# Kernel optimization log

Measured on AMD Instinct MI355X. Metric: run time of the kernel, lower is better.

## Reference

```python
import jax, jax.numpy as jnp
import numpy as np

B, S, C, H = 64, 512, 256, 128
P = S  # predict_length defaults to seq_length


def _linear_init(k, fan_in, fan_out):
    bound = 1.0 / np.sqrt(fan_in)
    kw, kb = jax.random.split(k)
    w = jax.random.uniform(kw, (fan_in, fan_out), minval=-bound, maxval=bound, dtype=jnp.float32)
    b = jax.random.uniform(kb, (fan_out,), minval=-bound, maxval=bound, dtype=jnp.float32)
    return w, b


def setup_inputs() -> dict:
    key = jax.random.key(0)
    ks = jax.random.split(key, 10)
    x = jax.random.normal(ks[0], (B, S, C), dtype=jnp.float32)
    wq1, bq1 = _linear_init(ks[1], S, H)
    wk1, bk1 = _linear_init(ks[2], S, H)
    wq2, bq2 = _linear_init(ks[3], S // 2, H)
    wk2, bk2 = _linear_init(ks[4], S // 2, H)
    wq3, bq3 = _linear_init(ks[5], S // 4, H)
    wk3, bk3 = _linear_init(ks[6], S // 4, H)
    wv, bv = _linear_init(ks[7], S, S)
    wo, bo = _linear_init(ks[8], S, P)
    return dict(x=x, wq1=wq1, bq1=bq1, wk1=wk1, bk1=bk1,
                wq2=wq2, bq2=bq2, wk2=wk2, bk2=bk2,
                wq3=wq3, bq3=bq3, wk3=wk3, bk3=bk3,
                wv=wv, bv=bv, wo=wo, bo=bo)


def _channel_attn(xl, wq, bq, wk, bk):
    # xl: [b', C, L]; q,k: [b', C, H]; returns softmax channel-attention [b', C, C]
    q = xl @ wq + bq
    k = xl @ wk + bk
    scores = jnp.einsum('bch,bdh->bcd', q, k) / jnp.sqrt(jnp.asarray(H, q.dtype))
    return jax.nn.softmax(scores, axis=-1)


def reference(x, wq1, bq1, wk1, bk1, wq2, bq2, wk2, bk2, wq3, bq3, wk3, bk3, wv, bv, wo, bo):
    b, s, c = x.shape
    x1 = jnp.swapaxes(x, -2, -1)                                   # [B, C, S]
    x2 = jnp.swapaxes(x.reshape(b * 2, s // 2, c), -2, -1)          # [2B, C, S/2]
    x3 = jnp.swapaxes(x.reshape(b * 4, s // 4, c), -2, -1)          # [4B, C, S/4]
    a1 = _channel_attn(x1, wq1, bq1, wk1, bk1)                      # [B, C, C]
    a2 = _channel_attn(x2, wq2, bq2, wk2, bk2).reshape(b, 2, c, c).mean(axis=1)
    a3 = _channel_attn(x3, wq3, bq3, wk3, bk3).reshape(b, 4, c, c).mean(axis=1)
    stacked = jnp.stack([a1, a2, a3], axis=0)                       # [3, B, C, C]
    gate = jax.nn.softmax(stacked, axis=0)                          # softmax over scales
    attn = (stacked * gate).sum(axis=0)                             # gated multi-scale combine [B, C, C]
    v = x1 @ wv + bv                                                # [B, C, S]
    out = (attn @ v) @ wo + bo                                      # [B, C, P]
    return jnp.swapaxes(out, -2, -1)                                # [B, P, C]
```

## Files before the change

### kernel.cpp

```cpp
#include <hip/hip_runtime.h>
#include <hip/hip_bf16.h>


typedef __attribute__((ext_vector_type(8))) short bf16x8;
typedef __attribute__((ext_vector_type(4))) float f32x4;
typedef __attribute__((ext_vector_type(8))) unsigned short ushort8;

typedef __attribute__((address_space(1))) void* as1vp;
typedef __attribute__((address_space(3))) void* as3vp;

__device__ __forceinline__ void gl2lds16(const void* g, void* l) {
  __builtin_amdgcn_global_load_lds((as1vp)(void*)g, (as3vp)l, 16, 0, 0);
}

__device__ __forceinline__ float bf2f(unsigned short u) {
  union { unsigned int i; float f; } v; v.i = ((unsigned int)u) << 16; return v.f;
}
__device__ __forceinline__ unsigned short f2bf(float f) {
  union { float f; unsigned int i; } v; v.f = f;
  unsigned int r = v.i + 0x7FFFu + ((v.i >> 16) & 1u);
  return (unsigned short)(r >> 16);
}
__device__ __forceinline__ unsigned long long pack4bf(float a, float b, float c, float d) {
  return (unsigned long long)f2bf(a) | ((unsigned long long)f2bf(b) << 16) |
         ((unsigned long long)f2bf(c) << 32) | ((unsigned long long)f2bf(d) << 48);
}

__global__ void __launch_bounds__(256) tcast_all(
    const float* __restrict__ x,
    const float* __restrict__ wq1, const float* __restrict__ wk1,
    const float* __restrict__ wq2, const float* __restrict__ wk2,
    const float* __restrict__ wq3, const float* __restrict__ wk3,
    const float* __restrict__ wv, const float* __restrict__ wo,
    unsigned short* __restrict__ XT,
    unsigned short* __restrict__ W1, unsigned short* __restrict__ W2,
    unsigned short* __restrict__ W3, unsigned short* __restrict__ WVNT,
    unsigned short* __restrict__ WOT) {
  const int bid = blockIdx.x;
  const int t = threadIdx.x;
  if (bid >= 2168) {
    long i0 = (long)(bid - 2168) * 2048 + t * 8;
    f32x4 a = *(const f32x4*)(wv + i0);
    f32x4 b = *(const f32x4*)(wv + i0 + 4);
    ushort8 o;
#pragma unroll
    for (int j = 0; j < 4; ++j) { o[j] = f2bf(a[j]); o[4 + j] = f2bf(b[j]); }
    *(ushort8*)(WVNT + i0) = o;
    return;
  }
  __shared__ float lds[64][68];
  const float* S; unsigned short* D; int R, Cc, r0, c0, rowoff = 0;
  if (bid < 2048) {
    int bz = bid >> 5, i = bid & 31;
    S = x + (long)bz * 131072; D = XT + (long)bz * 131072;
    R = 512; Cc = 256; r0 = (i & 7) * 64; c0 = (i >> 3) * 64;
  } else {
    int wb = bid - 2048;
    if (wb < 32) {
      int m = wb >> 4, i = wb & 15;
      S = m ? wk1 : wq1; D = W1; R = 512; Cc = 128;
      r0 = (i & 7) * 64; c0 = (i >> 3) * 64; rowoff = m * 128;
    } else if (wb < 48) {
      int m = (wb - 32) >> 3, i = (wb - 32) & 7;
      S = m ? wk2 : wq2; D = W2; R = 256; Cc = 128;
      r0 = (i & 3) * 64; c0 = (i >> 2) * 64; rowoff = m * 128;
    } else if (wb < 56) {
      int m = (wb - 48) >> 2, i = (wb - 48) & 3;
      S = m ? wk3 : wq3; D = W3; R = 128; Cc = 128;
      r0 = (i & 1) * 64; c0 = (i >> 1) * 64; rowoff = m * 128;
    } else {
      int i = wb - 56; S = wo; D = WOT; R = 512; Cc = 512;
      r0 = (i & 7) * 64; c0 = (i >> 3) * 64;
    }
  }
  {
    const int row = t >> 2, cq = (t & 3) * 16;
    const float* Sp = S + (long)(r0 + row) * Cc + c0 + cq;
#pragma unroll
    for (int j = 0; j < 4; ++j)
      *(f32x4*)&lds[row][cq + j * 4] = *(const f32x4*)(Sp + j * 4);
  }
  __syncthreads();
  {
    const int rq = (t & 15) * 4, ccb = t >> 4;
#pragma unroll
    for (int j = 0; j < 4; ++j) {
      int cc = ccb + j * 16;
      *(unsigned long long*)(D + (long)(c0 + cc + rowoff) * R + r0 + rq) =
          pack4bf(lds[rq][cc], lds[rq + 1][cc], lds[rq + 2][cc], lds[rq + 3][cc]);
    }
  }
}

__global__ void __launch_bounds__(512) projscore(
    const unsigned short* __restrict__ XT,
    const unsigned short* __restrict__ W1, const unsigned short* __restrict__ W2,
    const unsigned short* __restrict__ W3,
    const unsigned short* __restrict__ WOT, const unsigned short* __restrict__ WVNT,
    unsigned short* __restrict__ WVOT, float* __restrict__ BVO,
    const float* __restrict__ bv,
    unsigned short* __restrict__ A1F, unsigned short* __restrict__ A2F,
    unsigned short* __restrict__ A3F,
    const float* __restrict__ bq1, const float* __restrict__ bk1,
    const float* __restrict__ bq2, const float* __restrict__ bk2,
    const float* __restrict__ bq3, const float* __restrict__ bk3) {
  extern __shared__ char smem[];
  const int z = blockIdx.z;
  const int t = threadIdx.x, lane = t & 63, wid = t >> 6;

  if (z >= 464) {
    int p0 = (z - 464) * 128 + wid * 16;
    f32x4 b0 = *(const f32x4*)(bv + lane * 8);
    f32x4 b1 = *(const f32x4*)(bv + lane * 8 + 4);
#pragma unroll
    for (int i = 0; i < 16; ++i) {
      int p = p0 + i;
      bf16x8 wrow = *(const bf16x8*)(WOT + (long)p * 512 + lane * 8);
      float s = 0.0f;
#pragma unroll
      for (int j = 0; j < 4; ++j) {
        s += b0[j] * bf2f((unsigned short)wrow[j]);
        s += b1[j] * bf2f((unsigned short)wrow[4 + j]);
      }
#pragma unroll
      for (int off = 1; off < 64; off <<= 1) s += __shfl_xor(s, off, 64);
      if (lane == 0) BVO[p] = s;
    }
    return;
  }

  const int srow = t >> 3, ssl = t & 7;

  if (z >= 448) {
    const int w = z - 448;
    const int m0 = (w >> 2) * 128, n0 = (w & 3) * 128;
    const unsigned short* Ab = WOT + (long)m0 * 512;
    const unsigned short* Bb = WVNT + (long)n0 * 512;
    const int wmb = (wid >> 2) * 64, wnb = (wid & 3) * 32;
    f32x4 acc[4][2] = {};
    auto stageS = [&](int buf, int k0) {
      char* s = smem + buf * 32768;
#pragma unroll
      for (int i = 0; i < 2; ++i) {
        int row = i * 64 + srow;
        gl2lds16(Ab + (long)row * 512 + k0 + (ssl ^ (row & 7)) * 8, s + i * 8192 + t * 16);
        gl2lds16(Bb + (long)row * 512 + k0 + (ssl ^ (row & 7)) * 8, s + 16384 + i * 8192 + t * 16);
      }
    };
    stageS(0, 0);
    stageS(1, 64);
    for (int j = 0; j < 8; ++j) {
      if (j < 7) asm volatile("s_waitcnt vmcnt(4)" ::: "memory");
      else       asm volatile("s_waitcnt vmcnt(0)" ::: "memory");
      __builtin_amdgcn_s_barrier();
      if (j + 2 < 8) stageS((j + 2) % 3, (j + 2) * 64);
      const char* s = smem + (j % 3) * 32768;
#pragma unroll
      for (int kk = 0; kk < 2; ++kk) {
        const int slot = kk * 4 + (lane >> 4);
        bf16x8 af[4], bfr[2];
#pragma unroll
        for (int mi = 0; mi < 4; ++mi) {
          int row = wmb + mi * 16 + (lane & 15);
          af[mi] = *(const bf16x8*)(s + row * 128 + 16 * (slot ^ (row & 7)));
        }
#pragma unroll
        for (int ni = 0; ni < 2; ++ni) {
          int row = wnb + ni * 16 + (lane & 15);
          bfr[ni] = *(const bf16x8*)(s + 16384 + row * 128 + 16 * (slot ^ (row & 7)));
        }
#pragma unroll
        for (int mi = 0; mi < 4; ++mi)
#pragma unroll
          for (int ni = 0; ni < 2; ++ni)
            acc[mi][ni] = __builtin_amdgcn_mfma_f32_16x16x32_bf16(af[mi], bfr[ni], acc[mi][ni], 0, 0, 0);
      }
    }
#pragma unroll
    for (int ni = 0; ni < 2; ++ni) {
      int col = n0 + wnb + ni * 16 + (lane & 15);
#pragma unroll
      for (int mi = 0; mi < 4; ++mi) {
        int rowb = m0 + wmb + mi * 16 + (lane >> 4) * 4;
#pragma unroll
        for (int r = 0; r < 4; ++r)
          WVOT[(long)(rowb + r) * 512 + col] = f2bf(acc[mi][ni][r]);
      }
    }
    return;
  }

  const unsigned short* Ab; const unsigned short* Bw; unsigned short* AF;
  const float *bq, *bk; int K; long sb;
  if (z < 64) {
    K = 512; Bw = W1; AF = A1F; sb = z; bq = bq1; bk = bk1;
    Ab = XT + (long)z * 131072;
  } else if (z < 192) {
    int u = z - 64; K = 256; Bw = W2; AF = A2F; sb = u; bq = bq2; bk = bk2;
    Ab = XT + (long)(u >> 1) * 131072 + (u & 1) * 256;
  } else {
    int u = z - 192; K = 128; Bw = W3; AF = A3F; sb = u; bq = bq3; bk = bk3;
    Ab = XT + (long)(u >> 2) * 131072 + (u & 3) * 128;
  }
  const int wmb = (wid >> 1) * 64, wnb = (wid & 1) * 128;

  auto stage = [&](int buf, int k0) {
    char* s = smem + buf * 65536;
#pragma unroll
    for (int i = 0; i < 4; ++i) {
      int row = i * 64 + srow;
      int sc = (ssl ^ (row & 7)) * 8;
      gl2lds16(Ab + (long)row * 512 + k0 + sc, s + i * 8192 + t * 16);
      gl2lds16(Bw + (long)row * K + k0 + sc, s + 32768 + i * 8192 + t * 16);
    }
  };

  f32x4 acc[4][8] = {};
  const int nst = K >> 6;
  stage(0, 0);
  __syncthreads();
  int cur = 0;
  for (int j = 0; j < nst; ++j) {
    if (j + 1 < nst) stage(cur ^ 1, (j + 1) * 64);
    const char* s = smem + cur * 65536;
#pragma unroll
    for (int kk = 0; kk < 2; ++kk) {
      const int slot = kk * 4 + (lane >> 4);
      bf16x8 af[4], bfr[8];
#pragma unroll
      for (int mi = 0; mi < 4; ++mi) {
        int row = wmb + mi * 16 + (lane & 15);
        af[mi] = *(const bf16x8*)(s + row * 128 + 16 * (slot ^ (row & 7)));
      }
#pragma unroll
      for (int ni = 0; ni < 8; ++ni) {
        int row = wnb + ni * 16 + (lane & 15);
        bfr[ni] = *(const bf16x8*)(s + 32768 + row * 128 + 16 * (slot ^ (row & 7)));
      }
#pragma unroll
      for (int mi = 0; mi < 4; ++mi)
#pragma unroll
        for (int ni = 0; ni < 8; ++ni)
          acc[mi][ni] = __builtin_amdgcn_mfma_f32_16x16x32_bf16(bfr[ni], af[mi], acc[mi][ni], 0, 0, 0);
    }
    __syncthreads();
    cur ^= 1;
  }

  {
    const int chB = (wid & 1) ? 65536 : 0;
    const float* bias = (wid & 1) ? bk : bq;
#pragma unroll
    for (int mi = 0; mi < 4; ++mi) {
      int rowm = wmb + mi * 16 + (lane & 15);
#pragma unroll
      for (int ni = 0; ni < 8; ++ni) {
        int h = ni * 16 + (lane >> 4) * 4;
        int addr = chB + (h >> 6) * 32768 + rowm * 128 +
                   16 * ((((h & 63) >> 3)) ^ (rowm & 7)) + (h & 7) * 2;
        *(unsigned long long*)(smem + addr) =
            pack4bf(acc[mi][ni][0] + bias[h], acc[mi][ni][1] + bias[h + 1],
                    acc[mi][ni][2] + bias[h + 2], acc[mi][ni][3] + bias[h + 3]);
      }
    }
  }
  __syncthreads();

  f32x4 acc2[2][16] = {};
#pragma unroll
  for (int kc = 0; kc < 2; ++kc)
#pragma unroll
    for (int kk = 0; kk < 2; ++kk) {
      const int slot = kk * 4 + (lane >> 4);
      bf16x8 qf[2];
#pragma unroll
      for (int m2 = 0; m2 < 2; ++m2) {
        int qrow = wid * 32 + m2 * 16 + (lane & 15);
        qf[m2] = *(const bf16x8*)(smem + kc * 32768 + qrow * 128 + 16 * (slot ^ (qrow & 7)));
      }
#pragma unroll
      for (int ni = 0; ni < 16; ++ni) {
        int krow = ni * 16 + (lane & 15);
        bf16x8 kf = *(const bf16x8*)(smem + 65536 + kc * 32768 + krow * 128 + 16 * (slot ^ (krow & 7)));
        acc2[0][ni] = __builtin_amdgcn_mfma_f32_16x16x32_bf16(qf[0], kf, acc2[0][ni], 0, 0, 0);
        acc2[1][ni] = __builtin_amdgcn_mfma_f32_16x16x32_bf16(qf[1], kf, acc2[1][ni], 0, 0, 0);
      }
    }

  const float sc = 0.088388347648318447f;
#pragma unroll
  for (int m2 = 0; m2 < 2; ++m2) {
    int quad = (2 * wid + m2) & 3;
    int m0idx = (2 * wid + m2) >> 2;
    unsigned short* Of = AF + ((sb * 4 + m0idx) * 256 + quad * 64 + lane) * 64;
#pragma unroll
    for (int r = 0; r < 4; ++r) {
      float mx = -1e30f;
#pragma unroll
      for (int ni = 0; ni < 16; ++ni) mx = fmaxf(mx, acc2[m2][ni][r]);
#pragma unroll
      for (int off = 1; off < 16; off <<= 1) mx = fmaxf(mx, __shfl_xor(mx, off, 64));
      float s = 0.0f;
#pragma unroll
      for (int ni = 0; ni < 16; ++ni) {
        float p = __expf((acc2[m2][ni][r] - mx) * sc);
        acc2[m2][ni][r] = p;
        s += p;
      }
#pragma unroll
      for (int off = 1; off < 16; off <<= 1) s += __shfl_xor(s, off, 64);
      float inv = 1.0f / s;
      ushort8 lo, hi;
#pragma unroll
      for (int j = 0; j < 8; ++j) {
        lo[j] = f2bf(acc2[m2][j][r] * inv);
        hi[j] = f2bf(acc2[m2][8 + j][r] * inv);
      }
      *(ushort8*)(Of + r * 16) = lo;
      *(ushort8*)(Of + r * 16 + 8) = hi;
    }
  }
}

__global__ void __launch_bounds__(256) gate_frag(
    const unsigned short* __restrict__ A1F, const unsigned short* __restrict__ A2F,
    const unsigned short* __restrict__ A3F, unsigned short* __restrict__ ATTN) {
  const long gid = (long)blockIdx.x * 256 + threadIdx.x;
  const long i = gid * 8;
  const int b = (int)(i >> 16);
  const int rest = (int)(i & 65535);
  ushort8 a1 = *(const ushort8*)(A1F + i);
  const long i2 = ((long)(2 * b) << 16) + rest;
  ushort8 a2a = *(const ushort8*)(A2F + i2);
  ushort8 a2b = *(const ushort8*)(A2F + i2 + 65536);
  const long i3 = ((long)(4 * b) << 16) + rest;
  ushort8 a3a = *(const ushort8*)(A3F + i3);
  ushort8 a3b = *(const ushort8*)(A3F + i3 + 65536);
  ushort8 a3c = *(const ushort8*)(A3F + i3 + 131072);
  ushort8 a3d = *(const ushort8*)(A3F + i3 + 196608);
  const int f = rest & 63;
  const int tl = (rest >> 6) & 255;
  const int m0idx = rest >> 14;
  const int quad = (tl >> 6) & 3;
  const int lane_s = tl & 63;
  const int r = f >> 4;
  const int u0 = f & 15;
  const int row = m0idx * 64 + quad * 16 + (lane_s >> 4) * 4 + r;
  unsigned short* Orow = ATTN + ((long)b << 16) + (long)row * 256 + (lane_s & 15);
#pragma unroll
  for (int j = 0; j < 8; ++j) {
    float A1 = bf2f(a1[j]);
    float A2 = 0.5f * (bf2f(a2a[j]) + bf2f(a2b[j]));
    float A3 = 0.25f * (bf2f(a3a[j]) + bf2f(a3b[j]) + bf2f(a3c[j]) + bf2f(a3d[j]));
    float m = fmaxf(A1, fmaxf(A2, A3));
    float e1 = __expf(A1 - m), e2 = __expf(A2 - m), e3 = __expf(A3 - m);
    Orow[(u0 + j) * 16] = f2bf((A1 * e1 + A2 * e2 + A3 * e3) / (e1 + e2 + e3));
  }
}

template <int F32OUT, int BIASMODE>
__global__ void __launch_bounds__(512) gemm8(
    const unsigned short* __restrict__ A, const unsigned short* __restrict__ B,
    void* __restrict__ OutV, const float* __restrict__ bias,
    int lda, int ldb, int K, long astr, long bstr, long ostr, int ldo) {
  extern __shared__ char smem[];
  const int t = threadIdx.x, lane = t & 63, wid = t >> 6;
  const int wmb = (wid >> 1) * 64, wnb = (wid & 1) * 64;
  const int m0 = blockIdx.y * 256, n0 = blockIdx.x * 128;
  const int bz = blockIdx.z;
  const unsigned short* Ab = A + (long)bz * astr + (long)m0 * lda;
  const unsigned short* Bb = B + (long)bz * bstr + (long)n0 * ldb;
  const int srow = t >> 3, ssl = t & 7;

  auto stage = [&](int buf, int k0) {
    char* s = smem + buf * 49152;
#pragma unroll
    for (int i = 0; i < 4; ++i) {
      int row = i * 64 + srow;
      gl2lds16(Ab + (long)row * lda + k0 + (ssl ^ (row & 7)) * 8, s + i * 8192 + t * 16);
    }
#pragma unroll
    for (int i = 0; i < 2; ++i) {
      int row = i * 64 + srow;
      gl2lds16(Bb + (long)row * ldb + k0 + (ssl ^ (row & 7)) * 8,
               s + 32768 + i * 8192 + t * 16);
    }
  };

  f32x4 acc[4][4] = {};
  const int nst = K >> 6;
  stage(0, 0);
  stage(1, 64);
  for (int j = 0; j < nst; ++j) {
    if (j + 1 < nst) asm volatile("s_waitcnt vmcnt(6)" ::: "memory");
    else             asm volatile("s_waitcnt vmcnt(0)" ::: "memory");
    __builtin_amdgcn_s_barrier();
    if (j + 2 < nst) stage((j + 2) % 3, (j + 2) * 64);
    const char* s = smem + (j % 3) * 49152;
#pragma unroll
    for (int kk = 0; kk < 2; ++kk) {
      const int slot = kk * 4 + (lane >> 4);
      bf16x8 af[4], bfr[4];
#pragma unroll
      for (int mi = 0; mi < 4; ++mi) {
        int row = wmb + mi * 16 + (lane & 15);
        af[mi] = *(const bf16x8*)(s + row * 128 + 16 * (slot ^ (row & 7)));
      }
#pragma unroll
      for (int ni = 0; ni < 4; ++ni) {
        int row = wnb + ni * 16 + (lane & 15);
        bfr[ni] = *(const bf16x8*)(s + 32768 + row * 128 + 16 * (slot ^ (row & 7)));
      }
#pragma unroll
      for (int mi = 0; mi < 4; ++mi)
#pragma unroll
        for (int ni = 0; ni < 4; ++ni)
          acc[mi][ni] = __builtin_amdgcn_mfma_f32_16x16x32_bf16(af[mi], bfr[ni], acc[mi][ni], 0, 0, 0);
    }
  }
#pragma unroll
  for (int mi = 0; mi < 4; ++mi) {
    int rowb = m0 + wmb + mi * 16 + (lane >> 4) * 4;
    float rb[4];
#pragma unroll
    for (int r = 0; r < 4; ++r) rb[r] = (BIASMODE == 2) ? bias[rowb + r] : 0.0f;
#pragma unroll
    for (int ni = 0; ni < 4; ++ni) {
      int col = n0 + wnb + ni * 16 + (lane & 15);
#pragma unroll
      for (int r = 0; r < 4; ++r) {
        float v = acc[mi][ni][r] + rb[r];
        if constexpr (F32OUT)
          ((float*)OutV)[(long)bz * ostr + (long)(rowb + r) * ldo + col] = v;
        else
          ((unsigned short*)OutV)[(long)bz * ostr + (long)(rowb + r) * ldo + col] = f2bf(v);
      }
    }
  }
}

extern "C" void kernel_launch(void* const* d_in, const int* in_sizes, int n_in,
                              void* d_out, int out_size, void* d_ws, size_t ws_size,
                              hipStream_t stream) {
  (void)in_sizes; (void)n_in; (void)out_size; (void)ws_size;
  const float* x   = (const float*)d_in[0];
  const float* wq1 = (const float*)d_in[1];
  const float* bq1 = (const float*)d_in[2];
  const float* wk1 = (const float*)d_in[3];
  const float* bk1 = (const float*)d_in[4];
  const float* wq2 = (const float*)d_in[5];
  const float* bq2 = (const float*)d_in[6];
  const float* wk2 = (const float*)d_in[7];
  const float* bk2 = (const float*)d_in[8];
  const float* wq3 = (const float*)d_in[9];
  const float* bq3 = (const float*)d_in[10];
  const float* wk3 = (const float*)d_in[11];
  const float* bk3 = (const float*)d_in[12];
  const float* wv  = (const float*)d_in[13];
  const float* bv  = (const float*)d_in[14];
  const float* wo  = (const float*)d_in[15];
  const float* bo  = (const float*)d_in[16];
  char* ws = (char*)d_ws;

  unsigned short* XT   = (unsigned short*)(ws + 0);
  unsigned short* WQK1 = (unsigned short*)(ws + 16777216);
  unsigned short* WQK2 = (unsigned short*)(ws + 17039360);
  unsigned short* WQK3 = (unsigned short*)(ws + 17170432);
  unsigned short* WOT  = (unsigned short*)(ws + 17235968);
  unsigned short* WVNT = (unsigned short*)(ws + 17760256);
  unsigned short* WVOT = (unsigned short*)(ws + 18284544);
  float*          BVO  = (float*)(ws + 18808832);
  unsigned short* A1F  = (unsigned short*)(ws + 18876416);
  unsigned short* A2F  = (unsigned short*)(ws + 27265024);
  unsigned short* A3F  = (unsigned short*)(ws + 44042240);
  unsigned short* ATTN = (unsigned short*)(ws + 77596672);
  unsigned short* XVT  = (unsigned short*)(ws + 18876416);

  tcast_all<<<dim3(2296), dim3(256), 0, stream>>>(
      x, wq1, wk1, wq2, wk2, wq3, wk3, wv, wo,
      XT, WQK1, WQK2, WQK3, WVNT, WOT);

  projscore<<<dim3(1, 1, 468), dim3(512), 131072, stream>>>(
      XT, WQK1, WQK2, WQK3, WOT, WVNT, WVOT, BVO, bv,
      A1F, A2F, A3F, bq1, bk1, bq2, bk2, bq3, bk3);

  gate_frag<<<dim3(2048), dim3(256), 0, stream>>>(A1F, A2F, A3F, ATTN);

  gemm8<0, 2><<<dim3(2, 2, 64), dim3(512), 147456, stream>>>(
      WVOT, XT, XVT, BVO, 512, 512, 512, 0, 131072, 131072, 256);
  gemm8<1, 2><<<dim3(2, 2, 64), dim3(512), 147456, stream>>>(
      XVT, ATTN, d_out, bo, 256, 256, 256, 131072, 65536, 131072, 256);
}
```

Before: 95.48 us.

## Load B-operand fragments directly from global memory instead of staging through LDS

In the projscore kernel paths and in gemm8, the B operand is no longer copied into shared memory. Each lane reads its bf16x8 MFMA fragment straight from global memory (served by L1/L2), and the LDS buffers and waitcnt counts shrink to match. The goal is to halve LDS traffic and footprint, which could allow more blocks per CU. The cost is direct global loads in the inner loop whose latency is not hidden by the async prefetch pipeline, and the access pattern is poorly coalesced.

```diff
diff --git a/kernel.cpp b/kernel.cpp
--- a/kernel.cpp
+++ b/kernel.cpp
@@ -139,22 +139,19 @@
     const int wmb = (wid >> 2) * 64, wnb = (wid & 3) * 32;
     f32x4 acc[4][2] = {};
     auto stageS = [&](int buf, int k0) {
-      char* s = smem + buf * 32768;
+      char* s = smem + buf * 16384;
 #pragma unroll
       for (int i = 0; i < 2; ++i) {
         int row = i * 64 + srow;
         gl2lds16(Ab + (long)row * 512 + k0 + (ssl ^ (row & 7)) * 8, s + i * 8192 + t * 16);
-        gl2lds16(Bb + (long)row * 512 + k0 + (ssl ^ (row & 7)) * 8, s + 16384 + i * 8192 + t * 16);
       }
     };
     stageS(0, 0);
-    stageS(1, 64);
-    for (int j = 0; j < 8; ++j) {
-      if (j < 7) asm volatile("s_waitcnt vmcnt(4)" ::: "memory");
-      else       asm volatile("s_waitcnt vmcnt(0)" ::: "memory");
-      __builtin_amdgcn_s_barrier();
-      if (j + 2 < 8) stageS((j + 2) % 3, (j + 2) * 64);
-      const char* s = smem + (j % 3) * 32768;
+    __syncthreads();
+    int cur = 0;
+    for (int k0 = 0; k0 < 512; k0 += 64) {
+      if (k0 + 64 < 512) stageS(cur ^ 1, k0 + 64);
+      const char* s = smem + cur * 16384;
 #pragma unroll
       for (int kk = 0; kk < 2; ++kk) {
         const int slot = kk * 4 + (lane >> 4);
@@ -167,7 +164,7 @@
 #pragma unroll
         for (int ni = 0; ni < 2; ++ni) {
           int row = wnb + ni * 16 + (lane & 15);
-          bfr[ni] = *(const bf16x8*)(s + 16384 + row * 128 + 16 * (slot ^ (row & 7)));
+          bfr[ni] = *(const bf16x8*)(Bb + (long)row * 512 + k0 + slot * 8);
         }
 #pragma unroll
         for (int mi = 0; mi < 4; ++mi)
@@ -175,6 +172,8 @@
           for (int ni = 0; ni < 2; ++ni)
             acc[mi][ni] = __builtin_amdgcn_mfma_f32_16x16x32_bf16(af[mi], bfr[ni], acc[mi][ni], 0, 0, 0);
       }
+      __syncthreads();
+      cur ^= 1;
     }
 #pragma unroll
     for (int ni = 0; ni < 2; ++ni) {
@@ -205,13 +204,11 @@
   const int wmb = (wid >> 1) * 64, wnb = (wid & 1) * 128;
 
   auto stage = [&](int buf, int k0) {
-    char* s = smem + buf * 65536;
+    char* s = smem + buf * 32768;
 #pragma unroll
     for (int i = 0; i < 4; ++i) {
       int row = i * 64 + srow;
-      int sc = (ssl ^ (row & 7)) * 8;
-      gl2lds16(Ab + (long)row * 512 + k0 + sc, s + i * 8192 + t * 16);
-      gl2lds16(Bw + (long)row * K + k0 + sc, s + 32768 + i * 8192 + t * 16);
+      gl2lds16(Ab + (long)row * 512 + k0 + (ssl ^ (row & 7)) * 8, s + i * 8192 + t * 16);
     }
   };
 
@@ -222,7 +219,8 @@
   int cur = 0;
   for (int j = 0; j < nst; ++j) {
     if (j + 1 < nst) stage(cur ^ 1, (j + 1) * 64);
-    const char* s = smem + cur * 65536;
+    const int k0 = j * 64;
+    const char* s = smem + cur * 32768;
 #pragma unroll
     for (int kk = 0; kk < 2; ++kk) {
       const int slot = kk * 4 + (lane >> 4);
@@ -235,7 +233,7 @@
 #pragma unroll
       for (int ni = 0; ni < 8; ++ni) {
         int row = wnb + ni * 16 + (lane & 15);
-        bfr[ni] = *(const bf16x8*)(s + 32768 + row * 128 + 16 * (slot ^ (row & 7)));
+        bfr[ni] = *(const bf16x8*)(Bw + (long)row * K + k0 + slot * 8);
       }
 #pragma unroll
       for (int mi = 0; mi < 4; ++mi)
@@ -373,17 +371,11 @@
   const int srow = t >> 3, ssl = t & 7;
 
   auto stage = [&](int buf, int k0) {
-    char* s = smem + buf * 49152;
+    char* s = smem + buf * 32768;
 #pragma unroll
     for (int i = 0; i < 4; ++i) {
       int row = i * 64 + srow;
       gl2lds16(Ab + (long)row * lda + k0 + (ssl ^ (row & 7)) * 8, s + i * 8192 + t * 16);
-    }
-#pragma unroll
-    for (int i = 0; i < 2; ++i) {
-      int row = i * 64 + srow;
-      gl2lds16(Bb + (long)row * ldb + k0 + (ssl ^ (row & 7)) * 8,
-               s + 32768 + i * 8192 + t * 16);
     }
   };
 
@@ -392,11 +384,12 @@
   stage(0, 0);
   stage(1, 64);
   for (int j = 0; j < nst; ++j) {
-    if (j + 1 < nst) asm volatile("s_waitcnt vmcnt(6)" ::: "memory");
+    if (j + 1 < nst) asm volatile("s_waitcnt vmcnt(4)" ::: "memory");
     else             asm volatile("s_waitcnt vmcnt(0)" ::: "memory");
     __builtin_amdgcn_s_barrier();
     if (j + 2 < nst) stage((j + 2) % 3, (j + 2) * 64);
-    const char* s = smem + (j % 3) * 49152;
+    const int k0 = j * 64;
+    const char* s = smem + (j % 3) * 32768;
 #pragma unroll
     for (int kk = 0; kk < 2; ++kk) {
       const int slot = kk * 4 + (lane >> 4);
@@ -409,7 +402,7 @@
 #pragma unroll
       for (int ni = 0; ni < 4; ++ni) {
         int row = wnb + ni * 16 + (lane & 15);
-        bfr[ni] = *(const bf16x8*)(s + 32768 + row * 128 + 16 * (slot ^ (row & 7)));
+        bfr[ni] = *(const bf16x8*)(Bb + (long)row * ldb + k0 + slot * 8);
       }
 #pragma unroll
       for (int mi = 0; mi < 4; ++mi)
@@ -486,8 +479,8 @@
 
   gate_frag<<<dim3(2048), dim3(256), 0, stream>>>(A1F, A2F, A3F, ATTN);
 
-  gemm8<0, 2><<<dim3(2, 2, 64), dim3(512), 147456, stream>>>(
+  gemm8<0, 2><<<dim3(2, 2, 64), dim3(512), 98304, stream>>>(
       WVOT, XT, XVT, BVO, 512, 512, 512, 0, 131072, 131072, 256);
-  gemm8<1, 2><<<dim3(2, 2, 64), dim3(512), 147456, stream>>>(
+  gemm8<1, 2><<<dim3(2, 2, 64), dim3(512), 98304, stream>>>(
       XVT, ATTN, d_out, bo, 256, 256, 256, 131072, 65536, 131072, 256);
 }
```

Result: slower. 130.2 us (+36.4%).

## Run projscore with 1024-thread blocks to halve per-wave tiles and registers

Applied to the files above, without the earlier changes.

Doubles the projscore block to 16 waves and shrinks each wave's accumulator tiles (projection 4x4, score one 16-row strip, WV·WO subblock 2x2). The aim is more waves in flight per CU to hide MFMA and LDS latency, and lower register pressure per wave. The WV·WO path also loses its triple-buffered pipelined staging in favour of a single buffer with a barrier each k-step, which may expose load latency. Larger blocks also mean more costly barriers.

```diff
diff --git a/kernel.cpp b/kernel.cpp
--- a/kernel.cpp
+++ b/kernel.cpp
@@ -92,7 +92,7 @@
   }
 }
 
-__global__ void __launch_bounds__(512) projscore(
+__global__ void __launch_bounds__(1024) projscore(
     const unsigned short* __restrict__ XT,
     const unsigned short* __restrict__ W1, const unsigned short* __restrict__ W2,
     const unsigned short* __restrict__ W3,
@@ -109,11 +109,11 @@
   const int t = threadIdx.x, lane = t & 63, wid = t >> 6;
 
   if (z >= 464) {
-    int p0 = (z - 464) * 128 + wid * 16;
+    int p0 = (z - 464) * 128 + wid * 8;
     f32x4 b0 = *(const f32x4*)(bv + lane * 8);
     f32x4 b1 = *(const f32x4*)(bv + lane * 8 + 4);
 #pragma unroll
-    for (int i = 0; i < 16; ++i) {
+    for (int i = 0; i < 8; ++i) {
       int p = p0 + i;
       bf16x8 wrow = *(const bf16x8*)(WOT + (long)p * 512 + lane * 8);
       float s = 0.0f;
@@ -129,58 +129,47 @@
     return;
   }
 
-  const int srow = t >> 3, ssl = t & 7;
+  const int rS = t >> 3, sS = t & 7;
 
   if (z >= 448) {
     const int w = z - 448;
     const int m0 = (w >> 2) * 128, n0 = (w & 3) * 128;
     const unsigned short* Ab = WOT + (long)m0 * 512;
     const unsigned short* Bb = WVNT + (long)n0 * 512;
-    const int wmb = (wid >> 2) * 64, wnb = (wid & 3) * 32;
-    f32x4 acc[4][2] = {};
-    auto stageS = [&](int buf, int k0) {
-      char* s = smem + buf * 32768;
-#pragma unroll
-      for (int i = 0; i < 2; ++i) {
-        int row = i * 64 + srow;
-        gl2lds16(Ab + (long)row * 512 + k0 + (ssl ^ (row & 7)) * 8, s + i * 8192 + t * 16);
-        gl2lds16(Bb + (long)row * 512 + k0 + (ssl ^ (row & 7)) * 8, s + 16384 + i * 8192 + t * 16);
-      }
-    };
-    stageS(0, 0);
-    stageS(1, 64);
-    for (int j = 0; j < 8; ++j) {
-      if (j < 7) asm volatile("s_waitcnt vmcnt(4)" ::: "memory");
-      else       asm volatile("s_waitcnt vmcnt(0)" ::: "memory");
-      __builtin_amdgcn_s_barrier();
-      if (j + 2 < 8) stageS((j + 2) % 3, (j + 2) * 64);
-      const char* s = smem + (j % 3) * 32768;
+    const int wmb = (wid >> 2) * 32, wnb = (wid & 3) * 32;
+    f32x4 acc[2][2] = {};
+    for (int k0 = 0; k0 < 512; k0 += 64) {
+      int sc = (sS ^ (rS & 7)) * 8;
+      gl2lds16(Ab + (long)rS * 512 + k0 + sc, smem + t * 16);
+      gl2lds16(Bb + (long)rS * 512 + k0 + sc, smem + 16384 + t * 16);
+      __syncthreads();
 #pragma unroll
       for (int kk = 0; kk < 2; ++kk) {
         const int slot = kk * 4 + (lane >> 4);
-        bf16x8 af[4], bfr[2];
-#pragma unroll
-        for (int mi = 0; mi < 4; ++mi) {
+        bf16x8 af[2], bfr[2];
+#pragma unroll
+        for (int mi = 0; mi < 2; ++mi) {
           int row = wmb + mi * 16 + (lane & 15);
-          af[mi] = *(const bf16x8*)(s + row * 128 + 16 * (slot ^ (row & 7)));
+          af[mi] = *(const bf16x8*)(smem + row * 128 + 16 * (slot ^ (row & 7)));
         }
 #pragma unroll
         for (int ni = 0; ni < 2; ++ni) {
           int row = wnb + ni * 16 + (lane & 15);
-          bfr[ni] = *(const bf16x8*)(s + 16384 + row * 128 + 16 * (slot ^ (row & 7)));
+          bfr[ni] = *(const bf16x8*)(smem + 16384 + row * 128 + 16 * (slot ^ (row & 7)));
         }
 #pragma unroll
-        for (int mi = 0; mi < 4; ++mi)
+        for (int mi = 0; mi < 2; ++mi)
 #pragma unroll
           for (int ni = 0; ni < 2; ++ni)
             acc[mi][ni] = __builtin_amdgcn_mfma_f32_16x16x32_bf16(af[mi], bfr[ni], acc[mi][ni], 0, 0, 0);
       }
+      __syncthreads();
     }
 #pragma unroll
     for (int ni = 0; ni < 2; ++ni) {
       int col = n0 + wnb + ni * 16 + (lane & 15);
 #pragma unroll
-      for (int mi = 0; mi < 4; ++mi) {
+      for (int mi = 0; mi < 2; ++mi) {
         int rowb = m0 + wmb + mi * 16 + (lane >> 4) * 4;
 #pragma unroll
         for (int r = 0; r < 4; ++r)
@@ -202,20 +191,20 @@
     int u = z - 192; K = 128; Bw = W3; AF = A3F; sb = u; bq = bq3; bk = bk3;
     Ab = XT + (long)(u >> 2) * 131072 + (u & 3) * 128;
   }
-  const int wmb = (wid >> 1) * 64, wnb = (wid & 1) * 128;
+  const int wmb = (wid >> 2) * 64, wnb = (wid & 3) * 64;
 
   auto stage = [&](int buf, int k0) {
     char* s = smem + buf * 65536;
 #pragma unroll
-    for (int i = 0; i < 4; ++i) {
-      int row = i * 64 + srow;
-      int sc = (ssl ^ (row & 7)) * 8;
-      gl2lds16(Ab + (long)row * 512 + k0 + sc, s + i * 8192 + t * 16);
-      gl2lds16(Bw + (long)row * K + k0 + sc, s + 32768 + i * 8192 + t * 16);
+    for (int i = 0; i < 2; ++i) {
+      int row = i * 128 + rS;
+      int sc = (sS ^ (row & 7)) * 8;
+      gl2lds16(Ab + (long)row * 512 + k0 + sc, s + i * 16384 + t * 16);
+      gl2lds16(Bw + (long)row * K + k0 + sc, s + 32768 + i * 16384 + t * 16);
     }
   };
 
-  f32x4 acc[4][8] = {};
+  f32x4 acc[4][4] = {};
   const int nst = K >> 6;
   stage(0, 0);
   __syncthreads();
@@ -226,21 +215,21 @@
 #pragma unroll
     for (int kk = 0; kk < 2; ++kk) {
       const int slot = kk * 4 + (lane >> 4);
-      bf16x8 af[4], bfr[8];
+      bf16x8 af[4], bfr[4];
 #pragma unroll
       for (int mi = 0; mi < 4; ++mi) {
         int row = wmb + mi * 16 + (lane & 15);
         af[mi] = *(const bf16x8*)(s + row * 128 + 16 * (slot ^ (row & 7)));
       }
 #pragma unroll
-      for (int ni = 0; ni < 8; ++ni) {
+      for (int ni = 0; ni < 4; ++ni) {
         int row = wnb + ni * 16 + (lane & 15);
         bfr[ni] = *(const bf16x8*)(s + 32768 + row * 128 + 16 * (slot ^ (row & 7)));
       }
 #pragma unroll
       for (int mi = 0; mi < 4; ++mi)
 #pragma unroll
-        for (int ni = 0; ni < 8; ++ni)
+        for (int ni = 0; ni < 4; ++ni)
           acc[mi][ni] = __builtin_amdgcn_mfma_f32_16x16x32_bf16(bfr[ni], af[mi], acc[mi][ni], 0, 0, 0);
     }
     __syncthreads();
@@ -248,16 +237,17 @@
   }
 
   {
-    const int chB = (wid & 1) ? 65536 : 0;
-    const float* bias = (wid & 1) ? bk : bq;
+    const int chB = (wnb < 128) ? 0 : 65536;
+    const float* bias = (wnb < 128) ? bq : bk;
+    const int hbase = wnb & 127;
 #pragma unroll
     for (int mi = 0; mi < 4; ++mi) {
       int rowm = wmb + mi * 16 + (lane & 15);
 #pragma unroll
-      for (int ni = 0; ni < 8; ++ni) {
-        int h = ni * 16 + (lane >> 4) * 4;
+      for (int ni = 0; ni < 4; ++ni) {
+        int h = hbase + ni * 16 + (lane >> 4) * 4;
         int addr = chB + (h >> 6) * 32768 + rowm * 128 +
-                   16 * ((((h & 63) >> 3)) ^ (rowm & 7)) + (h & 7) * 2;
+                   16 * (((h & 63) >> 3) ^ (rowm & 7)) + (h & 7) * 2;
         *(unsigned long long*)(smem + addr) =
             pack4bf(acc[mi][ni][0] + bias[h], acc[mi][ni][1] + bias[h + 1],
                     acc[mi][ni][2] + bias[h + 2], acc[mi][ni][3] + bias[h + 3]);
@@ -266,45 +256,38 @@
   }
   __syncthreads();
 
-  f32x4 acc2[2][16] = {};
+  f32x4 acc2[16] = {};
+  const int qrow = wid * 16 + (lane & 15);
 #pragma unroll
   for (int kc = 0; kc < 2; ++kc)
 #pragma unroll
     for (int kk = 0; kk < 2; ++kk) {
       const int slot = kk * 4 + (lane >> 4);
-      bf16x8 qf[2];
-#pragma unroll
-      for (int m2 = 0; m2 < 2; ++m2) {
-        int qrow = wid * 32 + m2 * 16 + (lane & 15);
-        qf[m2] = *(const bf16x8*)(smem + kc * 32768 + qrow * 128 + 16 * (slot ^ (qrow & 7)));
-      }
+      bf16x8 qf = *(const bf16x8*)(smem + kc * 32768 + qrow * 128 + 16 * (slot ^ (qrow & 7)));
 #pragma unroll
       for (int ni = 0; ni < 16; ++ni) {
         int krow = ni * 16 + (lane & 15);
         bf16x8 kf = *(const bf16x8*)(smem + 65536 + kc * 32768 + krow * 128 + 16 * (slot ^ (krow & 7)));
-        acc2[0][ni] = __builtin_amdgcn_mfma_f32_16x16x32_bf16(qf[0], kf, acc2[0][ni], 0, 0, 0);
-        acc2[1][ni] = __builtin_amdgcn_mfma_f32_16x16x32_bf16(qf[1], kf, acc2[1][ni], 0, 0, 0);
+        acc2[ni] = __builtin_amdgcn_mfma_f32_16x16x32_bf16(qf, kf, acc2[ni], 0, 0, 0);
       }
     }
 
   const float sc = 0.088388347648318447f;
-#pragma unroll
-  for (int m2 = 0; m2 < 2; ++m2) {
-    int quad = (2 * wid + m2) & 3;
-    int m0idx = (2 * wid + m2) >> 2;
+  {
+    int m0idx = wid >> 2, quad = wid & 3;
     unsigned short* Of = AF + ((sb * 4 + m0idx) * 256 + quad * 64 + lane) * 64;
 #pragma unroll
     for (int r = 0; r < 4; ++r) {
       float mx = -1e30f;
 #pragma unroll
-      for (int ni = 0; ni < 16; ++ni) mx = fmaxf(mx, acc2[m2][ni][r]);
+      for (int ni = 0; ni < 16; ++ni) mx = fmaxf(mx, acc2[ni][r]);
 #pragma unroll
       for (int off = 1; off < 16; off <<= 1) mx = fmaxf(mx, __shfl_xor(mx, off, 64));
       float s = 0.0f;
 #pragma unroll
       for (int ni = 0; ni < 16; ++ni) {
-        float p = __expf((acc2[m2][ni][r] - mx) * sc);
-        acc2[m2][ni][r] = p;
+        float p = __expf((acc2[ni][r] - mx) * sc);
+        acc2[ni][r] = p;
         s += p;
       }
 #pragma unroll
@@ -313,8 +296,8 @@
       ushort8 lo, hi;
 #pragma unroll
       for (int j = 0; j < 8; ++j) {
-        lo[j] = f2bf(acc2[m2][j][r] * inv);
-        hi[j] = f2bf(acc2[m2][8 + j][r] * inv);
+        lo[j] = f2bf(acc2[j][r] * inv);
+        hi[j] = f2bf(acc2[8 + j][r] * inv);
       }
       *(ushort8*)(Of + r * 16) = lo;
       *(ushort8*)(Of + r * 16 + 8) = hi;
@@ -480,7 +463,7 @@
       x, wq1, wk1, wq2, wk2, wq3, wk3, wv, wo,
       XT, WQK1, WQK2, WQK3, WVNT, WOT);
 
-  projscore<<<dim3(1, 1, 468), dim3(512), 131072, stream>>>(
+  projscore<<<dim3(1, 1, 468), dim3(1024), 131072, stream>>>(
       XT, WQK1, WQK2, WQK3, WOT, WVNT, WVOT, BVO, bv,
       A1F, A2F, A3F, bq1, bk1, bq2, bk2, bq3, bk3);
 
```

Result: no change. 95.30 us (-0.2%).
